# Performance work log

Hardware: AMD Instinct MI355X
Metric: run time of the kernel (lower is better)

Reference implementation:

```python
import jax, jax.numpy as jnp
import numpy as np
from jax import lax

# PyTorch LSTM cell: gate order i, f, g, o; bias_ih + bias_hh folded into one b.
def _cell(carry, x, Wih, Whh, b):
    h, c = carry
    g = x @ Wih.T + h @ Whh.T + b
    i, f, gg, o = jnp.split(g, 4, axis=-1)
    c = jax.nn.sigmoid(f) * c + jax.nn.sigmoid(i) * jnp.tanh(gg)
    h = jax.nn.sigmoid(o) * jnp.tanh(c)
    return (h, c), h

def _bidir_layer(x_seq, Wih, Whh, b):
    # x_seq: [S, B, D]; Wih: [2, 4H, D] (dir 0 = fwd, 1 = bwd)
    B = x_seq.shape[1]
    H = Whh.shape[-1]
    z0 = (jnp.zeros((B, H), x_seq.dtype), jnp.zeros((B, H), x_seq.dtype))
    (hf, cf), of = lax.scan(lambda ca, x: _cell(ca, x, Wih[0], Whh[0], b[0]), z0, x_seq)
    (hb, cb), ob = lax.scan(lambda ca, x: _cell(ca, x, Wih[1], Whh[1], b[1]), z0, x_seq[::-1])
    out = jnp.concatenate([of, ob[::-1]], axis=-1)  # [S, B, 2H], time-aligned
    return out, (hf, cf), (hb, cb)


def setup_inputs() -> dict:
    key = jax.random.key(0)
    ks = jax.random.split(key, 26)
    V, E, H, S, B, T = 50000, 300, 512, 400, 32, 15
    def rn(k, shape, s=0.05):
        return (jax.random.normal(k, shape, jnp.float32) * s)
    return {
        "article": jax.random.randint(ks[0], (S, B), 0, V),
        "summary": jax.random.randint(ks[1], (T, B), 0, V),
        "z_noise": jax.random.normal(ks[2], (B, H), jnp.float32),
        "enc_emb": rn(ks[3], (V, E), 0.1),
        "enc_l0_Wih": rn(ks[4], (2, 4 * H, E)),
        "enc_l0_Whh": rn(ks[5], (2, 4 * H, H)),
        "enc_l0_b": rn(ks[6], (2, 4 * H)),
        "enc_l1_Wih": rn(ks[7], (2, 4 * H, 2 * H)),
        "enc_l1_Whh": rn(ks[8], (2, 4 * H, H)),
        "enc_l1_b": rn(ks[9], (2, 4 * H)),
        "mu_W": rn(ks[10], (H, H)),
        "mu_b": rn(ks[11], (H,)),
        "lv_W": rn(ks[12], (H, H)),
        "lv_b": rn(ks[13], (H,)),
        "dec_hid_W": rn(ks[14], (H, H)),
        "dec_hid_b": rn(ks[15], (H,)),
        "dec_emb": rn(ks[16], (V, E), 0.1),
        "dec_l0_Wih": rn(ks[17], (2, 4 * H, E)),
        "dec_l0_Whh": rn(ks[18], (2, 4 * H, H)),
        "dec_l0_b": rn(ks[19], (2, 4 * H)),
        "dec_l1_Wih": rn(ks[20], (2, 4 * H, 2 * H)),
        "dec_l1_Whh": rn(ks[21], (2, 4 * H, H)),
        "dec_l1_b": rn(ks[22], (2, 4 * H)),
        "pred_W": rn(ks[23], (V, 2 * H)),
        "pred_b": rn(ks[24], (V,)),
    }


def reference(article, summary, z_noise, enc_emb,
              enc_l0_Wih, enc_l0_Whh, enc_l0_b,
              enc_l1_Wih, enc_l1_Whh, enc_l1_b,
              mu_W, mu_b, lv_W, lv_b,
              dec_hid_W, dec_hid_b, dec_emb,
              dec_l0_Wih, dec_l0_Whh, dec_l0_b,
              dec_l1_Wih, dec_l1_Whh, dec_l1_b,
              pred_W, pred_b):
    # ---- encoder: embedding + 2-layer bidirectional LSTM ----
    emb = enc_emb[article]  # [S, B, E]
    o0, (h0f, c0f), (h0b, c0b) = _bidir_layer(emb, enc_l0_Wih, enc_l0_Whh, enc_l0_b)
    o1, (h1f, c1f), (h1b, c1b) = _bidir_layer(o0, enc_l1_Wih, enc_l1_Whh, enc_l1_b)
    hid = jnp.stack([h0f, h0b, h1f, h1b])   # [4, B, H] (torch layout l0f,l0b,l1f,l1b)
    c_enc = jnp.stack([c0f, c0b, c1f, c1b])

    # ---- VAE reparameterization ----
    mu = hid @ mu_W.T + mu_b            # [4, B, H]
    logvar = hid @ lv_W.T + lv_b
    z = z_noise * jnp.exp(0.5 * logvar) + mu  # broadcast [B,H] -> [4,B,H]

    # ---- decoder: greedy argmax feedback loop (self.tf is None) ----
    h_init = z @ dec_hid_W.T + dec_hid_b  # [4, B, H]

    def step(carry, _):
        dec_in, h, c = carry
        x = dec_emb[dec_in]  # [B, E]
        (h0f_, c0f_), _o = _cell((h[0], c[0]), x, dec_l0_Wih[0], dec_l0_Whh[0], dec_l0_b[0])
        (h0b_, c0b_), _o = _cell((h[1], c[1]), x, dec_l0_Wih[1], dec_l0_Whh[1], dec_l0_b[1])
        x1 = jnp.concatenate([h0f_, h0b_], axis=-1)  # [B, 2H]
        (h1f_, c1f_), _o = _cell((h[2], c[2]), x1, dec_l1_Wih[0], dec_l1_Whh[0], dec_l1_b[0])
        (h1b_, c1b_), _o = _cell((h[3], c[3]), x1, dec_l1_Wih[1], dec_l1_Whh[1], dec_l1_b[1])
        out = jnp.concatenate([h1f_, h1b_], axis=-1)  # [B, 2H]
        p = jax.nn.log_softmax(out @ pred_W.T + pred_b, axis=1)  # [B, V]
        h_new = jnp.stack([h0f_, h0b_, h1f_, h1b_])
        c_new = jnp.stack([c0f_, c0b_, c1f_, c1b_])
        return (jnp.argmax(p, axis=1), h_new, c_new), p

    T = summary.shape[0]
    _, outs = lax.scan(step, (summary[0], h_init, c_enc), None, length=T)  # [T, B, V]
    return (outs, mu, logvar, z)
```

## Files before the change

### kernel.cpp

```cpp
#include <hip/hip_runtime.h>
#include <math.h>

typedef _Float16 f16;
typedef __attribute__((__ext_vector_type__(8))) _Float16 f16x8;
typedef __attribute__((__ext_vector_type__(4))) float f32x4;
typedef __attribute__((__ext_vector_type__(2))) float fv2;

static __device__ __forceinline__ f32x4 mfma16(f16x8 a, f16x8 b, f32x4 c) {
  return __builtin_amdgcn_mfma_f32_16x16x32_f16(a, b, c, 0, 0, 0);
}
static __device__ __forceinline__ float sigf(float x) { return 1.0f / (1.0f + expf(-x)); }
static __device__ __forceinline__ void split2(float v, f16* hi, f16* lo) {
  f16 h = (f16)v;
  *hi = h;
  *lo = (f16)((v - (float)h) * 2048.0f);
}
static __device__ __forceinline__ unsigned packh(f16 a, f16 b) {
  union { f16 f; unsigned short u; } ua, ub;
  ua.f = a; ub.f = b;
  return (unsigned)ua.u | ((unsigned)ub.u << 16);
}
union H4 { f16 f[4]; uint2 u; };

struct Seg {
  const float* src; const int* idx; f16* hi; f16* lo;
  long end;
  int cs, cd;
};
struct SegTab { Seg s[13]; };

__global__ void k_prep(SegTab tab, long total, unsigned* bar) {
  if (blockIdx.x == 0 && threadIdx.x < 256) {
    bar[threadIdx.x] = 0;
    bar[threadIdx.x + 256] = 0;
  }
  for (long pos = (long)blockIdx.x * 256 + threadIdx.x; pos < total;
       pos += (long)gridDim.x * 256) {
    long start = 0; int si = 0;
    while (pos >= tab.s[si].end) { start = tab.s[si].end; ++si; }
    const Seg g = tab.s[si];
    long local = pos - start;
    float v;
    if (g.cd == 320) {
      unsigned l32 = (unsigned)local;
      unsigned r = l32 / 320u, c = l32 - r * 320u;
      long row = g.idx ? (long)g.idx[r] : (long)r;
      v = (c < 300u) ? g.src[row * 300 + c] : 0.0f;
    } else {
      v = g.src[local];
    }
    split2(v, &g.hi[local], &g.lo[local]);
  }
}

template <int BM>
__global__ __launch_bounds__(256, 1) void k_gemm(
    const f16* __restrict__ Ahi, const f16* __restrict__ Alo,
    const f16* __restrict__ Bhi, const f16* __restrict__ Blo,
    const float* __restrict__ bias, float* __restrict__ C,
    int M, int N, int K, long aB, long bB, long cB) {
  constexpr int MF = (BM == 128) ? 4 : 2;
  constexpr int NF = (BM == 128) ? 4 : 2;
  constexpr int ACH = BM * 8 / 256;
  __shared__ f16 sA[2][BM][72];
  __shared__ f16 sB[2][128][72];

  const int tid = threadIdx.x;
  const int wid = tid >> 6, lane = tid & 63;
  const int ln = lane & 15, l4 = lane >> 4;
  const int m0 = blockIdx.y * BM;
  const int n0 = blockIdx.x * 128;
  const int z = blockIdx.z;
  const f16* pA[2] = {Ahi + (long)z * aB, Alo + (long)z * aB};
  const f16* pB[2] = {Bhi + (long)z * bB, Blo + (long)z * bB};
  float* pC = C + (long)z * cB;

  const int wrow = (BM == 128) ? (wid >> 1) * 64 : 0;
  const int wcol = (BM == 128) ? (wid & 1) * 64 : wid * 32;

  f32x4 am[MF][NF], ax[MF][NF];
#pragma unroll
  for (int i = 0; i < MF; ++i)
#pragma unroll
    for (int j = 0; j < NF; ++j) {
      am[i][j] = (f32x4){0.f, 0.f, 0.f, 0.f};
      ax[i][j] = (f32x4){0.f, 0.f, 0.f, 0.f};
    }

  uint4 ra[2][ACH], rb[2][4];
  auto load_regs = [&](int k0) {
#pragma unroll
    for (int p = 0; p < 2; ++p) {
#pragma unroll
      for (int q = 0; q < ACH; ++q) {
        const int i = tid + q * 256;
        const int r = i >> 3, ch = i & 7;
        const int gr = m0 + r;
        uint4 v = make_uint4(0u, 0u, 0u, 0u);
        if (gr < M) v = *(const uint4*)(pA[p] + (long)gr * K + k0 + ch * 8);
        ra[p][q] = v;
      }
#pragma unroll
      for (int q = 0; q < 4; ++q) {
        const int i = tid + q * 256;
        const int r = i >> 3, ch = i & 7;
        const int gn = n0 + r;
        uint4 v = make_uint4(0u, 0u, 0u, 0u);
        if (gn < N) v = *(const uint4*)(pB[p] + (long)gn * K + k0 + ch * 8);
        rb[p][q] = v;
      }
    }
  };

  load_regs(0);
  for (int k0 = 0; k0 < K; k0 += 64) {
    __syncthreads();
#pragma unroll
    for (int p = 0; p < 2; ++p) {
#pragma unroll
      for (int q = 0; q < ACH; ++q) {
        const int i = tid + q * 256;
        *(uint4*)&sA[p][i >> 3][(i & 7) * 8] = ra[p][q];
      }
#pragma unroll
      for (int q = 0; q < 4; ++q) {
        const int i = tid + q * 256;
        *(uint4*)&sB[p][i >> 3][(i & 7) * 8] = rb[p][q];
      }
    }
    __syncthreads();
    if (k0 + 64 < K) load_regs(k0 + 64);
#pragma unroll
    for (int kk = 0; kk < 64; kk += 32) {
      const int kc = kk + l4 * 8;
      f16x8 ah[MF], al[MF], bh[NF], bl[NF];
#pragma unroll
      for (int i = 0; i < MF; ++i) {
        ah[i] = *(const f16x8*)&sA[0][wrow + i * 16 + ln][kc];
        al[i] = *(const f16x8*)&sA[1][wrow + i * 16 + ln][kc];
      }
#pragma unroll
      for (int j = 0; j < NF; ++j) {
        bh[j] = *(const f16x8*)&sB[0][wcol + j * 16 + ln][kc];
        bl[j] = *(const f16x8*)&sB[1][wcol + j * 16 + ln][kc];
      }
#pragma unroll
      for (int i = 0; i < MF; ++i)
#pragma unroll
        for (int j = 0; j < NF; ++j) {
          am[i][j] = mfma16(ah[i], bh[j], am[i][j]);
          ax[i][j] = mfma16(ah[i], bl[j], ax[i][j]);
          ax[i][j] = mfma16(al[i], bh[j], ax[i][j]);
        }
    }
  }
#pragma unroll
  for (int i = 0; i < MF; ++i)
#pragma unroll
    for (int j = 0; j < NF; ++j) {
      int row = m0 + wrow + i * 16 + l4 * 4;
      int col = n0 + wcol + j * 16 + ln;
      if (col < N) {
        float bv = bias ? bias[col] : 0.0f;
#pragma unroll
        for (int r = 0; r < 4; ++r)
          if (row + r < M)
            pC[(long)(row + r) * N + col] = am[i][j][r] + ax[i][j][r] * (1.0f / 2048.0f) + bv;
      }
    }
}

__global__ __launch_bounds__(256, 1) void k_lstm(
    const f16* __restrict__ WhhHi, const f16* __restrict__ WhhLo,
    const float* __restrict__ Gx,
    f16* __restrict__ hHi, f16* __restrict__ hLo,
    f16* __restrict__ oHi, f16* __restrict__ oLo,
    float* __restrict__ hidOut, f16* __restrict__ hidOutH, f16* __restrict__ hidOutL,
    float* __restrict__ cOut,
    unsigned* __restrict__ bar, int S, int layer) {
  const int tid = threadIdx.x;
  const int d = blockIdx.x >> 5;
  const int wg = blockIdx.x & 31;
  const int j0 = wg * 16;

  __shared__ f16 sHh[32][520];
  __shared__ f16 sHl[32][520];
  __shared__ float sGate[2][4][32][16];

  const int wid = tid >> 6, lane = tid & 63;
  const int gh = wid & 1, kh = wid >> 1;
  const int ln = lane & 15, lk8 = (lane >> 4) * 8;

  f16x8 wbh[2][8], wbl[2][8];
#pragma unroll
  for (int gl = 0; gl < 2; ++gl) {
    const long rowb = ((long)d * 2048 + (gh * 2 + gl) * 512 + j0 + ln) << 9;
#pragma unroll
    for (int ks = 0; ks < 8; ++ks) {
      const long off = rowb + (kh * 8 + ks) * 32 + lk8;
      wbh[gl][ks] = *(const f16x8*)(WhhHi + off);
      wbl[gl][ks] = *(const f16x8*)(WhhLo + off);
    }
  }

  unsigned* flags = bar + d * 64;
  const unsigned* myFlag = flags + (tid & 31);
  const int cb = tid >> 3;
  const int cj = (tid & 7) * 2;
  float creg0 = 0.0f, creg1 = 0.0f;

  {
    long zo = ((long)d * 32 + cb) * 512 + j0 + cj;
    unsigned zero = 0;
    char* zh = (char*)(hHi + zo);
    char* zl = (char*)(hLo + zo);
    asm volatile("global_store_dword %0, %1, off sc0 sc1" ::"v"(zh), "v"(zero) : "memory");
    asm volatile("global_store_dword %0, %1, off sc0 sc1" ::"v"(zl), "v"(zero) : "memory");
    asm volatile("s_waitcnt vmcnt(0) lgkmcnt(0)" ::: "memory");
    __builtin_amdgcn_s_barrier();
    if (tid == 0) {
      unsigned one = 1u;
      asm volatile("global_store_dword %0, %1, off sc0 sc1" ::"v"(flags + wg), "v"(one)
                   : "memory");
    }
    for (;;) {
      unsigned v;
      asm volatile("global_load_dword %0, %1, off sc0 sc1" : "=v"(v) : "v"(myFlag) : "memory");
      asm volatile("s_waitcnt vmcnt(0)" ::: "memory");
      if (__all(v >= 1u)) break;
      __builtin_amdgcn_s_sleep(1);
    }
    __builtin_amdgcn_sched_barrier(0);
  }

  for (int t = 0; t < S; ++t) {
    const int trow = d ? (S - 1 - t) : t;
    const int par = t & 1;

    uint4 hv[16];
    {
      const char* hb = (const char*)(hHi + ((long)par * 2 + d) * 32 * 512);
      const char* lb = (const char*)(hLo + ((long)par * 2 + d) * 32 * 512);
#pragma unroll
      for (int q = 0; q < 8; ++q) {
        const char* p = hb + (((long)q * 256 + tid) << 4);
        asm volatile("global_load_dwordx4 %0, %1, off sc0 sc1" : "=v"(hv[q]) : "v"(p));
      }
#pragma unroll
      for (int q = 0; q < 8; ++q) {
        const char* p = lb + (((long)q * 256 + tid) << 4);
        asm volatile("global_load_dwordx4 %0, %1, off sc0 sc1" : "=v"(hv[8 + q]) : "v"(p));
      }
    }
    fv2 gxv[4];
#pragma unroll
    for (int g = 0; g < 4; ++g) {
      const char* p = (const char*)&Gx[((long)trow * 32 + cb) * 4096 + (long)d * 2048 +
                                       g * 512 + j0 + cj];
      asm volatile("global_load_dwordx2 %0, %1, off" : "=v"(gxv[g]) : "v"(p));
    }
    asm volatile("s_waitcnt vmcnt(4)" ::: "memory");
    __builtin_amdgcn_sched_barrier(0);
#pragma unroll
    for (int q = 0; q < 8; ++q) {
      int c = q * 256 + tid;
      *(uint4*)&sHh[c >> 6][(c & 63) * 8] = hv[q];
      *(uint4*)&sHl[c >> 6][(c & 63) * 8] = hv[8 + q];
    }
    asm volatile("s_waitcnt lgkmcnt(0)" ::: "memory");
    __builtin_amdgcn_s_barrier();

    f32x4 am[2][2], ax[2][2];
#pragma unroll
    for (int a = 0; a < 2; ++a)
#pragma unroll
      for (int b2 = 0; b2 < 2; ++b2) {
        am[a][b2] = (f32x4){0.f, 0.f, 0.f, 0.f};
        ax[a][b2] = (f32x4){0.f, 0.f, 0.f, 0.f};
      }
#pragma unroll
    for (int ks = 0; ks < 8; ++ks) {
      const int kc = (kh * 8 + ks) * 32 + lk8;
      f16x8 a0h = *(const f16x8*)&sHh[ln][kc];
      f16x8 a1h = *(const f16x8*)&sHh[16 + ln][kc];
      f16x8 a0l = *(const f16x8*)&sHl[ln][kc];
      f16x8 a1l = *(const f16x8*)&sHl[16 + ln][kc];
#pragma unroll
      for (int gl = 0; gl < 2; ++gl) {
        am[gl][0] = mfma16(a0h, wbh[gl][ks], am[gl][0]);
        ax[gl][0] = mfma16(a0h, wbl[gl][ks], ax[gl][0]);
        ax[gl][0] = mfma16(a0l, wbh[gl][ks], ax[gl][0]);
        am[gl][1] = mfma16(a1h, wbh[gl][ks], am[gl][1]);
        ax[gl][1] = mfma16(a1h, wbl[gl][ks], ax[gl][1]);
        ax[gl][1] = mfma16(a1l, wbh[gl][ks], ax[gl][1]);
      }
    }

#pragma unroll
    for (int gl = 0; gl < 2; ++gl) {
      const int g = gh * 2 + gl;
#pragma unroll
      for (int mf = 0; mf < 2; ++mf) {
        const int row = mf * 16 + (lane >> 4) * 4;
#pragma unroll
        for (int r = 0; r < 4; ++r)
          sGate[kh][g][row + r][ln] = am[gl][mf][r] + ax[gl][mf][r] * (1.0f / 2048.0f);
      }
    }
    asm volatile("s_waitcnt lgkmcnt(0)" ::: "memory");
    __builtin_amdgcn_s_barrier();

    asm volatile("s_waitcnt vmcnt(0)" ::: "memory");
    __builtin_amdgcn_sched_barrier(0);

    {
      float i0 = sGate[0][0][cb][cj] + sGate[1][0][cb][cj] + gxv[0][0];
      float i1 = sGate[0][0][cb][cj + 1] + sGate[1][0][cb][cj + 1] + gxv[0][1];
      float f0 = sGate[0][1][cb][cj] + sGate[1][1][cb][cj] + gxv[1][0];
      float f1 = sGate[0][1][cb][cj + 1] + sGate[1][1][cb][cj + 1] + gxv[1][1];
      float g0 = sGate[0][2][cb][cj] + sGate[1][2][cb][cj] + gxv[2][0];
      float g1 = sGate[0][2][cb][cj + 1] + sGate[1][2][cb][cj + 1] + gxv[2][1];
      float o0 = sGate[0][3][cb][cj] + sGate[1][3][cb][cj] + gxv[3][0];
      float o1 = sGate[0][3][cb][cj + 1] + sGate[1][3][cb][cj + 1] + gxv[3][1];
      float c0 = sigf(f0) * creg0 + sigf(i0) * tanhf(g0);
      float c1 = sigf(f1) * creg1 + sigf(i1) * tanhf(g1);
      creg0 = c0; creg1 = c1;
      float h0 = sigf(o0) * tanhf(c0);
      float h1 = sigf(o1) * tanhf(c1);
      f16 h0h, h0l, h1h, h1l;
      split2(h0, &h0h, &h0l);
      split2(h1, &h1h, &h1l);
      unsigned phi = packh(h0h, h1h), plo = packh(h0l, h1l);
      long ho = ((((long)(par ^ 1) * 2 + d) * 32 + cb) * 512 + j0 + cj);
      char* dh = (char*)(hHi + ho);
      char* dl = (char*)(hLo + ho);
      asm volatile("global_store_dword %0, %1, off sc0 sc1" ::"v"(dh), "v"(phi) : "memory");
      asm volatile("global_store_dword %0, %1, off sc0 sc1" ::"v"(dl), "v"(plo) : "memory");
      if (oHi) {
        long oo = ((long)trow * 32 + cb) * 1024 + (long)d * 512 + j0 + cj;
        *(unsigned*)(oHi + oo) = phi;
        *(unsigned*)(oLo + oo) = plo;
      }
      if (t == S - 1) {
        long so = (((long)layer * 2 + d) * 32 + cb) * 512 + j0 + cj;
        *(float2*)(hidOut + so) = make_float2(h0, h1);
        *(unsigned*)(hidOutH + so) = phi;
        *(unsigned*)(hidOutL + so) = plo;
        *(float2*)(cOut + so) = make_float2(c0, c1);
      }
    }

    asm volatile("s_waitcnt vmcnt(0) lgkmcnt(0)" ::: "memory");
    __builtin_amdgcn_s_barrier();
    const unsigned tg = (unsigned)t + 2u;
    if (tid == 0) {
      asm volatile("global_store_dword %0, %1, off sc0 sc1" ::"v"(flags + wg), "v"(tg)
                   : "memory");
    }
    for (;;) {
      unsigned v;
      asm volatile("global_load_dword %0, %1, off sc0 sc1" : "=v"(v) : "v"(myFlag) : "memory");
      asm volatile("s_waitcnt vmcnt(0)" ::: "memory");
      if (__all(v >= tg)) break;
      __builtin_amdgcn_s_sleep(1);
    }
    __builtin_amdgcn_sched_barrier(0);
  }
}

template <int XK, bool GATHER>
static __device__ __forceinline__ void dec_body(
    int sub, const int* __restrict__ tok, const float* __restrict__ emb,
    const f16* __restrict__ xH, const f16* __restrict__ xL,
    const f16* __restrict__ WihH, const f16* __restrict__ WihL,
    const f16* __restrict__ WhhH, const f16* __restrict__ WhhL,
    const float* __restrict__ bias,
    const f16* __restrict__ dhInH, const f16* __restrict__ dhInL,
    f16* __restrict__ dhOutH, f16* __restrict__ dhOutL,
    float* __restrict__ cDec, f16* __restrict__ xoH, f16* __restrict__ xoL,
    int layer, f16 (&sA)[2][32][72], f16 (&sB)[2][64][72], float (&sGate)[4][32][17]) {
  const int tid = threadIdx.x;
  const int d = sub >> 5;
  const int jt = sub & 31;
  const int s = layer * 2 + d;

  const int wid = tid >> 6, lane = tid & 63;
  const int ln = lane & 15, l4 = lane >> 4;
  const int ar = tid >> 3, ach = tid & 7;
  constexpr int NK = XK / 64 + 8;

  int tk = 0;
  if (GATHER) tk = tok[ar];

  f32x4 am[2], ax[2];
#pragma unroll
  for (int i = 0; i < 2; ++i) {
    am[i] = (f32x4){0.f, 0.f, 0.f, 0.f};
    ax[i] = (f32x4){0.f, 0.f, 0.f, 0.f};
  }

  uint4 ra0, ra1, rb[4];
  float gaf[8];

  auto load_regs = [&](int k) {
    const int k0 = k * 64;
    if (k0 < XK) {
      if (GATHER) {
        const float* rowp = emb + (long)tk * 300;
        const int c4 = k0 + ach * 8;
#pragma unroll
        for (int h = 0; h < 2; ++h) {
          float4 v = make_float4(0.f, 0.f, 0.f, 0.f);
          if (c4 + h * 4 < 300) v = *(const float4*)(rowp + c4 + h * 4);
          gaf[h * 4 + 0] = v.x; gaf[h * 4 + 1] = v.y;
          gaf[h * 4 + 2] = v.z; gaf[h * 4 + 3] = v.w;
        }
      } else {
        ra0 = *(const uint4*)(xH + (long)ar * XK + k0 + ach * 8);
        ra1 = *(const uint4*)(xL + (long)ar * XK + k0 + ach * 8);
      }
    } else {
      const int hk = k0 - XK;
      ra0 = *(const uint4*)(dhInH + ((long)s * 32 + ar) * 512 + hk + ach * 8);
      ra1 = *(const uint4*)(dhInL + ((long)s * 32 + ar) * 512 + hk + ach * 8);
    }
#pragma unroll
    for (int q = 0; q < 2; ++q) {
      const int i = tid + q * 256;
      const int r = i >> 3, ch = i & 7;
      const long srow = (long)d * 2048 + (r >> 4) * 512 + jt * 16 + (r & 15);
      if (k0 < XK) {
        rb[q * 2] = *(const uint4*)(WihH + srow * XK + k0 + ch * 8);
        rb[q * 2 + 1] = *(const uint4*)(WihL + srow * XK + k0 + ch * 8);
      } else {
        const int hk = k0 - XK;
        rb[q * 2] = *(const uint4*)(WhhH + srow * 512 + hk + ch * 8);
        rb[q * 2 + 1] = *(const uint4*)(WhhL + srow * 512 + hk + ch * 8);
      }
    }
  };

  load_regs(0);
  for (int k = 0; k < NK; ++k) {
    const bool gw = GATHER && (k * 64 < XK);
    __syncthreads();
    if (gw) {
#pragma unroll
      for (int u = 0; u < 8; ++u)
        split2(gaf[u], &sA[0][ar][ach * 8 + u], &sA[1][ar][ach * 8 + u]);
    } else {
      *(uint4*)&sA[0][ar][ach * 8] = ra0;
      *(uint4*)&sA[1][ar][ach * 8] = ra1;
    }
#pragma unroll
    for (int q = 0; q < 2; ++q) {
      const int i = tid + q * 256;
      const int r = i >> 3, ch = i & 7;
      *(uint4*)&sB[0][r][ch * 8] = rb[q * 2];
      *(uint4*)&sB[1][r][ch * 8] = rb[q * 2 + 1];
    }
    __syncthreads();
    if (k + 1 < NK) load_regs(k + 1);
#pragma unroll
    for (int kk = 0; kk < 64; kk += 32) {
      const int kc = kk + l4 * 8;
      f16x8 a0h = *(const f16x8*)&sA[0][ln][kc];
      f16x8 a1h = *(const f16x8*)&sA[0][16 + ln][kc];
      f16x8 a0l = *(const f16x8*)&sA[1][ln][kc];
      f16x8 a1l = *(const f16x8*)&sA[1][16 + ln][kc];
      f16x8 bh = *(const f16x8*)&sB[0][wid * 16 + ln][kc];
      f16x8 bl = *(const f16x8*)&sB[1][wid * 16 + ln][kc];
      am[0] = mfma16(a0h, bh, am[0]);
      ax[0] = mfma16(a0h, bl, ax[0]);
      ax[0] = mfma16(a0l, bh, ax[0]);
      am[1] = mfma16(a1h, bh, am[1]);
      ax[1] = mfma16(a1h, bl, ax[1]);
      ax[1] = mfma16(a1l, bh, ax[1]);
    }
  }

#pragma unroll
  for (int i2 = 0; i2 < 2; ++i2)
#pragma unroll
    for (int r = 0; r < 4; ++r)
      sGate[wid][i2 * 16 + l4 * 4 + r][ln] = am[i2][r] + ax[i2][r] * (1.0f / 2048.0f);
  __syncthreads();

  {
    const int b = tid >> 3, cj = (tid & 7) * 2;
    const int j = jt * 16 + cj;
    float iv0 = sGate[0][b][cj] + bias[d * 2048 + j];
    float iv1 = sGate[0][b][cj + 1] + bias[d * 2048 + j + 1];
    float fv0 = sGate[1][b][cj] + bias[d * 2048 + 512 + j];
    float fv1 = sGate[1][b][cj + 1] + bias[d * 2048 + 512 + j + 1];
    float gv0 = sGate[2][b][cj] + bias[d * 2048 + 1024 + j];
    float gv1 = sGate[2][b][cj + 1] + bias[d * 2048 + 1024 + j + 1];
    float ov0 = sGate[3][b][cj] + bias[d * 2048 + 1536 + j];
    float ov1 = sGate[3][b][cj + 1] + bias[d * 2048 + 1536 + j + 1];
    long co = ((long)s * 32 + b) * 512 + j;
    float2 cold = *(const float2*)&cDec[co];
    float c0 = sigf(fv0) * cold.x + sigf(iv0) * tanhf(gv0);
    float c1 = sigf(fv1) * cold.y + sigf(iv1) * tanhf(gv1);
    *(float2*)&cDec[co] = make_float2(c0, c1);
    float h0 = sigf(ov0) * tanhf(c0);
    float h1 = sigf(ov1) * tanhf(c1);
    f16 h0h, h0l, h1h, h1l;
    split2(h0, &h0h, &h0l);
    split2(h1, &h1h, &h1l);
    unsigned phi = packh(h0h, h1h), plo = packh(h0l, h1l);
    *(unsigned*)&dhOutH[co] = phi;
    *(unsigned*)&dhOutL[co] = plo;
    long xo = (long)b * 1024 + d * 512 + j;
    *(unsigned*)&xoH[xo] = phi;
    *(unsigned*)&xoL[xo] = plo;
  }
}

template <int XK, bool GATHER>
__global__ __launch_bounds__(256, 1) void k_dec(
    const int* __restrict__ tok, const float* __restrict__ emb,
    const f16* __restrict__ xH, const f16* __restrict__ xL,
    const f16* __restrict__ WihH, const f16* __restrict__ WihL,
    const f16* __restrict__ WhhH, const f16* __restrict__ WhhL,
    const float* __restrict__ bias,
    const f16* __restrict__ dhInH, const f16* __restrict__ dhInL,
    f16* __restrict__ dhOutH, f16* __restrict__ dhOutL,
    float* __restrict__ cDec, f16* __restrict__ xoH, f16* __restrict__ xoL,
    int layer) {
  __shared__ f16 sA[2][32][72];
  __shared__ f16 sB[2][64][72];
  __shared__ float sGate[4][32][17];
  dec_body<XK, GATHER>(blockIdx.x, tok, emb, xH, xL, WihH, WihL, WhhH, WhhL, bias,
                       dhInH, dhInL, dhOutH, dhOutL, cDec, xoH, xoL, layer, sA, sB,
                       sGate);
}

__global__ __launch_bounds__(256, 2) void k_pred(
    const f16* __restrict__ xH, const f16* __restrict__ xL,
    const f16* __restrict__ BH, const f16* __restrict__ BL,
    const float* __restrict__ bias, float* __restrict__ C) {
  __shared__ f16 sAh[32][520];
  __shared__ f16 sAl[32][520];
  const int tid = threadIdx.x;

  auto stageA = [&](int koff) {
#pragma unroll
    for (int q = 0; q < 8; ++q) {
      int idx = tid + q * 256;
      int r = idx >> 6, c8 = idx & 63;
      *(uint4*)&sAh[r][c8 * 8] = *(const uint4*)(xH + r * 1024 + koff + c8 * 8);
      *(uint4*)&sAl[r][c8 * 8] = *(const uint4*)(xL + r * 1024 + koff + c8 * 8);
    }
  };

  const int wid = tid >> 6, lane = tid & 63;
  const int ln = lane & 15, l4 = lane >> 4;
  const int n0 = blockIdx.x * 128 + wid * 32;

  const int row0 = n0 + ln, row1 = n0 + 16 + ln;
  const f16* pbh0 = BH + (long)(row0 < 50000 ? row0 : 0) * 1024 + l4 * 8;
  const f16* pbl0 = BL + (long)(row0 < 50000 ? row0 : 0) * 1024 + l4 * 8;
  const f16* pbh1 = BH + (long)(row1 < 50000 ? row1 : 0) * 1024 + l4 * 8;
  const f16* pbl1 = BL + (long)(row1 < 50000 ? row1 : 0) * 1024 + l4 * 8;

  f32x4 am[2][2], ax[2][2];
#pragma unroll
  for (int i = 0; i < 2; ++i)
#pragma unroll
    for (int j = 0; j < 2; ++j) {
      am[i][j] = (f32x4){0.f, 0.f, 0.f, 0.f};
      ax[i][j] = (f32x4){0.f, 0.f, 0.f, 0.f};
    }

  f16x8 b0[4], b1[4], b2[4], b3[4];
  auto loadB = [&](int s, f16x8* buf) {
    const long o = (long)s * 32;
    buf[0] = *(const f16x8*)(pbh0 + o);
    buf[1] = *(const f16x8*)(pbl0 + o);
    buf[2] = *(const f16x8*)(pbh1 + o);
    buf[3] = *(const f16x8*)(pbl1 + o);
  };
  auto comp = [&](int s, const f16x8* buf) {
    const int kc = (s & 15) * 32 + l4 * 8;
    f16x8 a0h = *(const f16x8*)&sAh[ln][kc];
    f16x8 a1h = *(const f16x8*)&sAh[16 + ln][kc];
    f16x8 a0l = *(const f16x8*)&sAl[ln][kc];
    f16x8 a1l = *(const f16x8*)&sAl[16 + ln][kc];
    am[0][0] = mfma16(a0h, buf[0], am[0][0]);
    ax[0][0] = mfma16(a0h, buf[1], ax[0][0]);
    ax[0][0] = mfma16(a0l, buf[0], ax[0][0]);
    am[1][0] = mfma16(a1h, buf[0], am[1][0]);
    ax[1][0] = mfma16(a1h, buf[1], ax[1][0]);
    ax[1][0] = mfma16(a1l, buf[0], ax[1][0]);
    am[0][1] = mfma16(a0h, buf[2], am[0][1]);
    ax[0][1] = mfma16(a0h, buf[3], ax[0][1]);
    ax[0][1] = mfma16(a0l, buf[2], ax[0][1]);
    am[1][1] = mfma16(a1h, buf[2], am[1][1]);
    ax[1][1] = mfma16(a1h, buf[3], ax[1][1]);
    ax[1][1] = mfma16(a1l, buf[2], ax[1][1]);
  };

  stageA(0);
  loadB(0, b0);
  loadB(1, b1);
  loadB(2, b2);
  __syncthreads();
#pragma unroll
  for (int h = 0; h < 2; ++h) {
    if (h) {
      __syncthreads();
      stageA(512);
      __syncthreads();
    }
#pragma unroll 1
    for (int s = h * 16; s < h * 16 + 16; s += 4) {
      loadB(s + 3, b3);
      comp(s, b0);
      loadB(s + 4, b0);
      comp(s + 1, b1);
      loadB(s + 5, b1);
      comp(s + 2, b2);
      loadB(s + 6, b2);
      comp(s + 3, b3);
    }
  }

#pragma unroll
  for (int j = 0; j < 2; ++j) {
    const int col = n0 + j * 16 + ln;
    if (col < 50000) {
      const float bv = bias[col];
#pragma unroll
      for (int i = 0; i < 2; ++i)
#pragma unroll
        for (int r = 0; r < 4; ++r) {
          const int row = i * 16 + l4 * 4 + r;
          C[(long)row * 50000 + col] = am[i][j][r] + ax[i][j][r] * (1.0f / 2048.0f) + bv;
        }
    }
  }
}

__global__ void k_vae(const float* __restrict__ mlOut, const float* __restrict__ mub,
                      const float* __restrict__ lvb, const float* __restrict__ zn,
                      float* __restrict__ outMu, float* __restrict__ outLv,
                      float* __restrict__ outZ, f16* __restrict__ zHi,
                      f16* __restrict__ zLo) {
  int i = blockIdx.x * 256 + threadIdx.x;
  if (i >= 4 * 32 * 512) return;
  int bj = i & (32 * 512 - 1);
  int j = i & 511;
  float m = mlOut[i] + mub[j];
  float l = mlOut[65536 + i] + lvb[j];
  float z = zn[bj] * expf(0.5f * l) + m;
  outMu[i] = m;
  outLv[i] = l;
  outZ[i] = z;
  split2(z, &zHi[i], &zLo[i]);
}

__global__ void k_decinit(const float* __restrict__ hInit, const float* __restrict__ cEnc,
                          const int* __restrict__ summary, f16* __restrict__ dhHi,
                          f16* __restrict__ dhLo, float* __restrict__ cDec,
                          int* __restrict__ tok) {
  int i = blockIdx.x * 256 + threadIdx.x;
  if (i < 4 * 32 * 512) {
    split2(hInit[i], &dhHi[i], &dhLo[i]);
    cDec[i] = cEnc[i];
  }
  if (i < 32) tok[i] = summary[i];
}

__global__ __launch_bounds__(1024) void k_lsm(const float* __restrict__ logits,
                                              float* __restrict__ outs,
                                              int* __restrict__ tok, int t) {
  const int b = blockIdx.x;
  const int tid = threadIdx.x;
  const float* lg = logits + (long)b * 50000;
  float m = -INFINITY, s = 0.0f;
  int am = 0;
  for (int v = tid; v < 50000; v += 1024) {
    float x = lg[v];
    if (x > m) {
      s = s * expf(m - x) + 1.0f;
      m = x;
      am = v;
    } else {
      s += expf(x - m);
    }
  }
  __shared__ float sm[1024], ss[1024];
  __shared__ int sa[1024];
  sm[tid] = m; ss[tid] = s; sa[tid] = am;
  __syncthreads();
  for (int o = 512; o > 0; o >>= 1) {
    if (tid < o) {
      float m2 = sm[tid + o], s2 = ss[tid + o];
      int a2 = sa[tid + o];
      float m1 = sm[tid], s1 = ss[tid];
      int a1 = sa[tid];
      if (m2 > m1 || (m2 == m1 && a2 < a1)) {
        sm[tid] = m2; ss[tid] = s2 + s1 * expf(m1 - m2); sa[tid] = a2;
      } else {
        ss[tid] = s1 + s2 * expf(m2 - m1);
      }
    }
    __syncthreads();
  }
  float lse = sm[0] + logf(ss[0]);
  float* ob = outs + ((long)t * 32 + b) * 50000;
  for (int v = tid; v < 50000; v += 1024) ob[v] = lg[v] - lse;
  if (tid == 0) tok[b] = sa[0];
}

extern "C" void kernel_launch(void* const* d_in, const int* in_sizes, int n_in,
                              void* d_out, int out_size, void* d_ws, size_t ws_size,
                              hipStream_t stream) {
  const int* article = (const int*)d_in[0];
  const int* summary = (const int*)d_in[1];
  const float* z_noise = (const float*)d_in[2];
  const float* enc_emb = (const float*)d_in[3];
  const float* e0Wih = (const float*)d_in[4];
  const float* e0Whh = (const float*)d_in[5];
  const float* e0b = (const float*)d_in[6];
  const float* e1Wih = (const float*)d_in[7];
  const float* e1Whh = (const float*)d_in[8];
  const float* e1b = (const float*)d_in[9];
  const float* muW = (const float*)d_in[10];
  const float* mub = (const float*)d_in[11];
  const float* lvW = (const float*)d_in[12];
  const float* lvb = (const float*)d_in[13];
  const float* dhW = (const float*)d_in[14];
  const float* dhb = (const float*)d_in[15];
  const float* dec_emb = (const float*)d_in[16];
  const float* d0Wih = (const float*)d_in[17];
  const float* d0Whh = (const float*)d_in[18];
  const float* d0b = (const float*)d_in[19];
  const float* d1Wih = (const float*)d_in[20];
  const float* d1Whh = (const float*)d_in[21];
  const float* d1b = (const float*)d_in[22];
  const float* predW = (const float*)d_in[23];
  const float* predb = (const float*)d_in[24];
  float* out = (float*)d_out;
  (void)in_sizes; (void)n_in; (void)out_size; (void)ws_size;

  char* w = (char*)d_ws;
  size_t off = 0;
  auto alloc = [&](size_t bytes) -> void* {
    void* p = w + off;
    off += (bytes + 255) & ~(size_t)255;
    return p;
  };

  f16* e0WihH = (f16*)alloc(4096L * 320 * 2);
  f16* e0WihL = (f16*)alloc(4096L * 320 * 2);
  f16* e0WhhH = (f16*)alloc(4096L * 512 * 2);
  f16* e0WhhL = (f16*)alloc(4096L * 512 * 2);
  f16* e1WihH = (f16*)alloc(4096L * 1024 * 2);
  f16* e1WihL = (f16*)alloc(4096L * 1024 * 2);
  f16* e1WhhH = (f16*)alloc(4096L * 512 * 2);
  f16* e1WhhL = (f16*)alloc(4096L * 512 * 2);
  f16* d0WihH = (f16*)alloc(4096L * 320 * 2);
  f16* d0WihL = (f16*)alloc(4096L * 320 * 2);
  f16* d0WhhH = (f16*)alloc(4096L * 512 * 2);
  f16* d0WhhL = (f16*)alloc(4096L * 512 * 2);
  f16* d1WihH = (f16*)alloc(4096L * 1024 * 2);
  f16* d1WihL = (f16*)alloc(4096L * 1024 * 2);
  f16* d1WhhH = (f16*)alloc(4096L * 512 * 2);
  f16* d1WhhL = (f16*)alloc(4096L * 512 * 2);
  f16* mlWH = (f16*)alloc(2L * 262144 * 2);
  f16* mlWL = (f16*)alloc(2L * 262144 * 2);
  f16* dhWH = (f16*)alloc(512L * 512 * 2);
  f16* dhWL = (f16*)alloc(512L * 512 * 2);
  f16* predH = (f16*)alloc(50000L * 1024 * 2);
  f16* predL = (f16*)alloc(50000L * 1024 * 2);
  f16* embH = (f16*)alloc(12800L * 320 * 2);
  f16* embL = (f16*)alloc(12800L * 320 * 2);
  f16* o0H = (f16*)alloc(12800L * 1024 * 2);
  f16* o0L = (f16*)alloc(12800L * 1024 * 2);
  float* Gx = (float*)alloc(12800L * 4096 * 4);
  f16* hEncH = (f16*)alloc(2L * 2 * 32 * 512 * 2);
  f16* hEncL = (f16*)alloc(2L * 2 * 32 * 512 * 2);
  float* hid = (float*)alloc(128L * 512 * 4);
  float* cEnc = (float*)alloc(128L * 512 * 4);
  f16* hidH = (f16*)alloc(128L * 512 * 2);
  f16* hidL = (f16*)alloc(128L * 512 * 2);
  float* mlOut = (float*)alloc(2L * 65536 * 4);
  f16* zH = (f16*)alloc(128L * 512 * 2);
  f16* zL = (f16*)alloc(128L * 512 * 2);
  float* hInit = (float*)alloc(128L * 512 * 4);
  f16* dhH = (f16*)alloc(2L * 65536 * 2);
  f16* dhL = (f16*)alloc(2L * 65536 * 2);
  float* cDec = (float*)alloc(4L * 32 * 512 * 4);
  f16* x1H = (f16*)alloc(32L * 1024 * 2);
  f16* x1L = (f16*)alloc(32L * 1024 * 2);
  f16* x2H = (f16*)alloc(32L * 1024 * 2);
  f16* x2L = (f16*)alloc(32L * 1024 * 2);
  float* logits = (float*)alloc(32L * 50000 * 4);
  int* tok = (int*)alloc(256);
  unsigned* bar = (unsigned*)alloc(2048);

  SegTab tab;
  long cum = 0;
  int si = 0;
  auto seg = [&](const float* src, const int* idx, f16* hi, f16* lo, long rows, int cs,
                 int cd) {
    cum += rows * cd;
    tab.s[si++] = Seg{src, idx, hi, lo, cum, cs, cd};
  };
  seg(e0Wih, nullptr, e0WihH, e0WihL, 4096, 300, 320);
  seg(e0Whh, nullptr, e0WhhH, e0WhhL, 4096, 512, 512);
  seg(e1Wih, nullptr, e1WihH, e1WihL, 4096, 1024, 1024);
  seg(e1Whh, nullptr, e1WhhH, e1WhhL, 4096, 512, 512);
  seg(d0Wih, nullptr, d0WihH, d0WihL, 4096, 300, 320);
  seg(d0Whh, nullptr, d0WhhH, d0WhhL, 4096, 512, 512);
  seg(d1Wih, nullptr, d1WihH, d1WihL, 4096, 1024, 1024);
  seg(d1Whh, nullptr, d1WhhH, d1WhhL, 4096, 512, 512);
  seg(muW, nullptr, mlWH, mlWL, 512, 512, 512);
  seg(lvW, nullptr, mlWH + 262144, mlWL + 262144, 512, 512, 512);
  seg(dhW, nullptr, dhWH, dhWL, 512, 512, 512);
  seg(predW, nullptr, predH, predL, 50000, 1024, 1024);
  seg(enc_emb, article, embH, embL, 12800, 300, 320);
  k_prep<<<8192, 256, 0, stream>>>(tab, cum, bar);

  k_gemm<128><<<dim3(32, 100, 1), 256, 0, stream>>>(embH, embL, e0WihH, e0WihL, e0b, Gx,
                                                    12800, 4096, 320, 0, 0, 0);
  k_lstm<<<64, 256, 0, stream>>>(e0WhhH, e0WhhL, Gx, hEncH, hEncL, o0H, o0L, hid, hidH,
                                 hidL, cEnc, bar, 400, 0);
  k_gemm<128><<<dim3(32, 100, 1), 256, 0, stream>>>(o0H, o0L, e1WihH, e1WihL, e1b, Gx,
                                                    12800, 4096, 1024, 0, 0, 0);
  k_lstm<<<64, 256, 0, stream>>>(e1WhhH, e1WhhL, Gx, hEncH, hEncL, (f16*)nullptr,
                                 (f16*)nullptr, hid, hidH, hidL, cEnc, bar + 128, 400, 1);

  k_gemm<32><<<dim3(4, 4, 2), 256, 0, stream>>>(hidH, hidL, mlWH, mlWL,
                                                (const float*)nullptr, mlOut, 128, 512,
                                                512, 0, 262144, 65536);
  k_vae<<<256, 256, 0, stream>>>(mlOut, mub, lvb, z_noise, out + 24000000L,
                                 out + 24065536L, out + 24131072L, zH, zL);
  k_gemm<32><<<dim3(4, 4, 1), 256, 0, stream>>>(zH, zL, dhWH, dhWL, dhb, hInit, 128, 512,
                                                512, 0, 0, 0);
  k_decinit<<<256, 256, 0, stream>>>(hInit, cEnc, summary, dhH, dhL, cDec, tok);

  for (int t = 0; t < 15; ++t) {
    int par = t & 1;
    f16* dIH = dhH + (long)par * 65536;
    f16* dIL = dhL + (long)par * 65536;
    f16* dOH = dhH + (long)(par ^ 1) * 65536;
    f16* dOL = dhL + (long)(par ^ 1) * 65536;
    k_dec<320, true><<<64, 256, 0, stream>>>(tok, dec_emb, (const f16*)nullptr,
                                             (const f16*)nullptr, d0WihH, d0WihL, d0WhhH,
                                             d0WhhL, d0b, dIH, dIL, dOH, dOL, cDec, x1H,
                                             x1L, 0);
    k_dec<1024, false><<<64, 256, 0, stream>>>((const int*)nullptr, (const float*)nullptr,
                                               x1H, x1L, d1WihH, d1WihL, d1WhhH, d1WhhL,
                                               d1b, dIH, dIL, dOH, dOL, cDec, x2H, x2L,
                                               1);
    k_pred<<<391, 256, 0, stream>>>(x2H, x2L, predH, predL, predb, logits);
    k_lsm<<<32, 1024, 0, stream>>>(logits, out, tok, t);
  }
}
```

Measured before the change: 6.582 ms.

## Fuse decoder layer-0 and layer-1 kernels with an in-kernel grid flag barrier

Merges the two per-step decoder LSTM layer launches into one kernel of 64 workgroups. The layers are separated by a global-memory flag barrier, and the layer-1 input is read and written with coherent (sc0 sc1) loads and stores. This removes one kernel launch and the inter-kernel gap per decoder step, 15 steps in all. In exchange it relies on all 64 workgroups being co-resident and on flags in bar+256 that the prep kernel zeroes.

```diff
diff --git a/kernel.cpp b/kernel.cpp
--- a/kernel.cpp
+++ b/kernel.cpp
@@ -21,6 +21,10 @@
   return (unsigned)ua.u | ((unsigned)ub.u << 16);
 }
 union H4 { f16 f[4]; uint2 u; };
+
+static __device__ __forceinline__ void st_cg4(void* p, unsigned v) {
+  asm volatile("global_store_dword %0, %1, off sc0 sc1" ::"v"(p), "v"(v) : "memory");
+}
 
 struct Seg {
   const float* src; const int* idx; f16* hi; f16* lo;
@@ -368,7 +372,7 @@
   }
 }
 
-template <int XK, bool GATHER>
+template <int XK, bool GATHER, bool COH_IN, bool COH_OUT>
 static __device__ __forceinline__ void dec_body(
     int sub, const int* __restrict__ tok, const float* __restrict__ emb,
     const f16* __restrict__ xH, const f16* __restrict__ xL,
@@ -415,6 +419,11 @@
           gaf[h * 4 + 0] = v.x; gaf[h * 4 + 1] = v.y;
           gaf[h * 4 + 2] = v.z; gaf[h * 4 + 3] = v.w;
         }
+      } else if (COH_IN) {
+        const char* p0 = (const char*)(xH + (long)ar * XK + k0 + ach * 8);
+        const char* p1 = (const char*)(xL + (long)ar * XK + k0 + ach * 8);
+        asm volatile("global_load_dwordx4 %0, %1, off sc0 sc1" : "=v"(ra0) : "v"(p0));
+        asm volatile("global_load_dwordx4 %0, %1, off sc0 sc1" : "=v"(ra1) : "v"(p1));
       } else {
         ra0 = *(const uint4*)(xH + (long)ar * XK + k0 + ach * 8);
         ra1 = *(const uint4*)(xL + (long)ar * XK + k0 + ach * 8);
@@ -511,28 +520,61 @@
     *(unsigned*)&dhOutH[co] = phi;
     *(unsigned*)&dhOutL[co] = plo;
     long xo = (long)b * 1024 + d * 512 + j;
-    *(unsigned*)&xoH[xo] = phi;
-    *(unsigned*)&xoL[xo] = plo;
-  }
-}
-
-template <int XK, bool GATHER>
-__global__ __launch_bounds__(256, 1) void k_dec(
+    if (COH_OUT) {
+      st_cg4(&xoH[xo], phi);
+      st_cg4(&xoL[xo], plo);
+    } else {
+      *(unsigned*)&xoH[xo] = phi;
+      *(unsigned*)&xoL[xo] = plo;
+    }
+  }
+}
+
+__global__ __launch_bounds__(256, 1) void k_dec2(
     const int* __restrict__ tok, const float* __restrict__ emb,
-    const f16* __restrict__ xH, const f16* __restrict__ xL,
-    const f16* __restrict__ WihH, const f16* __restrict__ WihL,
-    const f16* __restrict__ WhhH, const f16* __restrict__ WhhL,
-    const float* __restrict__ bias,
+    const f16* __restrict__ d0WihH, const f16* __restrict__ d0WihL,
+    const f16* __restrict__ d0WhhH, const f16* __restrict__ d0WhhL,
+    const float* __restrict__ d0b,
+    const f16* __restrict__ d1WihH, const f16* __restrict__ d1WihL,
+    const f16* __restrict__ d1WhhH, const f16* __restrict__ d1WhhL,
+    const float* __restrict__ d1b,
     const f16* __restrict__ dhInH, const f16* __restrict__ dhInL,
     f16* __restrict__ dhOutH, f16* __restrict__ dhOutL,
-    float* __restrict__ cDec, f16* __restrict__ xoH, f16* __restrict__ xoL,
-    int layer) {
+    float* __restrict__ cDec,
+    f16* __restrict__ x1H, f16* __restrict__ x1L,
+    f16* __restrict__ x2H, f16* __restrict__ x2L,
+    unsigned* __restrict__ flags, int step) {
   __shared__ f16 sA[2][32][72];
   __shared__ f16 sB[2][64][72];
   __shared__ float sGate[4][32][17];
-  dec_body<XK, GATHER>(blockIdx.x, tok, emb, xH, xL, WihH, WihL, WhhH, WhhL, bias,
-                       dhInH, dhInL, dhOutH, dhOutL, cDec, xoH, xoL, layer, sA, sB,
-                       sGate);
+  const int tid = threadIdx.x;
+  const int sub = blockIdx.x;
+  const unsigned tg = (unsigned)step + 1u;
+  const unsigned* myFlag = flags + (tid & 63);
+
+  dec_body<320, true, false, true>(sub, tok, emb, (const f16*)nullptr,
+                                   (const f16*)nullptr, d0WihH, d0WihL, d0WhhH, d0WhhL,
+                                   d0b, dhInH, dhInL, dhOutH, dhOutL, cDec, x1H, x1L,
+                                   0, sA, sB, sGate);
+  asm volatile("s_waitcnt vmcnt(0) lgkmcnt(0)" ::: "memory");
+  __builtin_amdgcn_s_barrier();
+  if (tid == 0) {
+    asm volatile("global_store_dword %0, %1, off sc0 sc1" ::"v"(flags + sub), "v"(tg)
+                 : "memory");
+  }
+  for (;;) {
+    unsigned v;
+    asm volatile("global_load_dword %0, %1, off sc0 sc1" : "=v"(v) : "v"(myFlag) : "memory");
+    asm volatile("s_waitcnt vmcnt(0)" ::: "memory");
+    if (__all(v >= tg)) break;
+    __builtin_amdgcn_s_sleep(1);
+  }
+  __builtin_amdgcn_sched_barrier(0);
+
+  dec_body<1024, false, true, false>(sub, (const int*)nullptr, (const float*)nullptr,
+                                     x1H, x1L, d1WihH, d1WihL, d1WhhH, d1WhhL, d1b,
+                                     dhInH, dhInL, dhOutH, dhOutL, cDec, x2H, x2L,
+                                     1, sA, sB, sGate);
 }
 
 __global__ __launch_bounds__(256, 2) void k_pred(
@@ -847,14 +889,9 @@
     f16* dIL = dhL + (long)par * 65536;
     f16* dOH = dhH + (long)(par ^ 1) * 65536;
     f16* dOL = dhL + (long)(par ^ 1) * 65536;
-    k_dec<320, true><<<64, 256, 0, stream>>>(tok, dec_emb, (const f16*)nullptr,
-                                             (const f16*)nullptr, d0WihH, d0WihL, d0WhhH,
-                                             d0WhhL, d0b, dIH, dIL, dOH, dOL, cDec, x1H,
-                                             x1L, 0);
-    k_dec<1024, false><<<64, 256, 0, stream>>>((const int*)nullptr, (const float*)nullptr,
-                                               x1H, x1L, d1WihH, d1WihL, d1WhhH, d1WhhL,
-                                               d1b, dIH, dIL, dOH, dOL, cDec, x2H, x2L,
-                                               1);
+    k_dec2<<<64, 256, 0, stream>>>(tok, dec_emb, d0WihH, d0WihL, d0WhhH, d0WhhL, d0b,
+                                   d1WihH, d1WihL, d1WhhH, d1WhhL, d1b, dIH, dIL, dOH,
+                                   dOL, cDec, x1H, x1L, x2H, x2L, bar + 256, t);
     k_pred<<<391, 256, 0, stream>>>(x2H, x2L, predH, predL, predb, logits);
     k_lsm<<<32, 1024, 0, stream>>>(logits, out, tok, t);
   }
```

Result: slower. 6.790 ms (+3.2%).
